# Optimization experiments

Hardware: AMD Instinct MI355X
Metric: run time of the kernel (lower is better)

The kernel has to match this reference:

```python
import jax, jax.numpy as jnp
import numpy as np

V, S, D, H, L = 32000, 2048, 768, 12, 6
HD = D // H
EPS = 1e-5


def _sinusoidal_pe(s, d):
    pos = np.arange(s)[:, None].astype(np.float32)
    div = np.exp(np.arange(0, d, 2).astype(np.float32) * (-np.log(10000.0) / d))
    pe = np.zeros((s, d), dtype=np.float32)
    pe[:, 0::2] = np.sin(pos * div)
    pe[:, 1::2] = np.cos(pos * div)
    return jnp.asarray(pe)


def setup_inputs() -> dict:
    key = jax.random.key(0)
    ks = jax.random.split(key, 16)
    std = 0.02
    tok_emb = jax.random.normal(ks[0], (V, D), jnp.float32) * std
    tok_emb = tok_emb.at[1].set(0.0)  # padding_idx=1
    pos_enc = _sinusoidal_pe(S, D)
    attn_w = jax.random.normal(ks[1], (L, 3 * D, D), jnp.float32) * std
    attn_b = jnp.zeros((L, 3 * D), jnp.float32)
    proj_std = 0.02 / np.sqrt(2 * 6)
    proj_w = jax.random.normal(ks[2], (L, D, D), jnp.float32) * proj_std
    proj_b = jnp.zeros((L, D), jnp.float32)
    ln1_g = jnp.ones((L, D), jnp.float32); ln1_b = jnp.zeros((L, D), jnp.float32)
    ln2_g = jnp.ones((L, D), jnp.float32); ln2_b = jnp.zeros((L, D), jnp.float32)
    fc1_w = jax.random.normal(ks[3], (L, 4 * D, D), jnp.float32) * std
    fc1_b = jnp.zeros((L, 4 * D), jnp.float32)
    fc2_w = jax.random.normal(ks[4], (L, D, 4 * D), jnp.float32) * std
    fc2_b = jnp.zeros((L, D), jnp.float32)
    dec_w = jax.random.normal(ks[5], (V, D), jnp.float32) * std
    idx = jax.random.randint(ks[6], (2, S), 0, V)
    return dict(idx=idx, tok_emb=tok_emb, pos_enc=pos_enc, attn_w=attn_w,
                attn_b=attn_b, proj_w=proj_w, proj_b=proj_b, ln1_g=ln1_g,
                ln1_b=ln1_b, ln2_g=ln2_g, ln2_b=ln2_b, fc1_w=fc1_w,
                fc1_b=fc1_b, fc2_w=fc2_w, fc2_b=fc2_b, dec_w=dec_w)


def _ln(x, g, b):
    mu = jnp.mean(x, -1, keepdims=True)
    var = jnp.mean(jnp.square(x - mu), -1, keepdims=True)
    return (x - mu) * jax.lax.rsqrt(var + EPS) * g + b


def _forward(idx, tok_emb, pos_enc, attn_w, attn_b, proj_w, proj_b,
             ln1_g, ln1_b, ln2_g, ln2_b, fc1_w, fc1_b, fc2_w, fc2_b, dec_w):
    b, s = idx.shape
    x = tok_emb[idx] + pos_enc[:s]  # [b,s,d]
    for l in range(L):
        h = _ln(x, ln1_g[l], ln1_b[l])
        qkv = h @ attn_w[l].T + attn_b[l]
        q, k, v = jnp.split(qkv, 3, axis=-1)
        q = q.reshape(b, s, H, HD).transpose(0, 2, 1, 3)
        k = k.reshape(b, s, H, HD).transpose(0, 2, 1, 3)
        v = v.reshape(b, s, H, HD).transpose(0, 2, 1, 3)
        att = jnp.einsum('bhqd,bhkd->bhqk', q, k) * (1.0 / np.sqrt(HD))
        att = jax.nn.softmax(att, axis=-1)  # no causal mask in source
        y = jnp.einsum('bhqk,bhkd->bhqd', att, v)
        y = y.transpose(0, 2, 1, 3).reshape(b, s, D)
        x = x + (y @ proj_w[l].T + proj_b[l])
        h = _ln(x, ln2_g[l], ln2_b[l])
        h = jax.nn.gelu(h @ fc1_w[l].T + fc1_b[l])
        x = x + (h @ fc2_w[l].T + fc2_b[l])
    return x @ dec_w.T  # [b,s,V]


def reference(idx, tok_emb, pos_enc, attn_w, attn_b, proj_w, proj_b,
              ln1_g, ln1_b, ln2_g, ln2_b, fc1_w, fc1_b, fc2_w, fc2_b, dec_w):
    return _forward(idx, tok_emb, pos_enc, attn_w, attn_b, proj_w, proj_b,
                    ln1_g, ln1_b, ln2_g, ln2_b, fc1_w, fc1_b, fc2_w, fc2_b, dec_w)
```

## Files before the change

### kernel.cpp

```cpp
#include <hip/hip_runtime.h>
#include <hip/hip_bf16.h>
#include <stdint.h>


typedef unsigned short u16;
typedef __attribute__((ext_vector_type(8))) __bf16 bf16x8;
typedef __attribute__((ext_vector_type(4))) float f32x4;
typedef __attribute__((ext_vector_type(4))) unsigned int u32x4;
typedef __attribute__((ext_vector_type(4))) unsigned short u16x4;
typedef __attribute__((ext_vector_type(8))) unsigned short u16x8;

#define MFMA16(a, b, c) __builtin_amdgcn_mfma_f32_16x16x32_bf16((a), (b), (c), 0, 0, 0)

__device__ __forceinline__ float b2f(u16 u) {
  union { unsigned int i; float f; } x; x.i = ((unsigned int)u) << 16; return x.f;
}
__device__ __forceinline__ u16 f2b(float f) {
  union { float f; unsigned int i; } x; x.f = f;
  unsigned int r = x.i + 0x7fffu + ((x.i >> 16) & 1u);
  return (u16)(r >> 16);
}
__device__ __forceinline__ float gelu_f(float v) {
  const float t = 0.7978845608028654f * (v + 0.044715f * v * v * v);
  const float e = __expf(-2.f * fabsf(t));
  float th = (1.f - e) / (1.f + e);
  th = (t < 0.f) ? -th : th;
  return 0.5f * v * (1.f + th);
}
__device__ __forceinline__ void lds16(u16* l, const u16* g) {
  __builtin_amdgcn_global_load_lds(
      (const __attribute__((address_space(1))) unsigned int*)g,
      (__attribute__((address_space(3))) unsigned int*)l, 16, 0, 0);
}

__global__ __launch_bounds__(256) void conv_bf16_kernel(
    const float* __restrict__ src, u16* __restrict__ dst, int n8) {
  int i = blockIdx.x * 256 + threadIdx.x;
  const int stride = gridDim.x * 256;
  for (; i < n8; i += stride) {
    const f32x4 a = *(const f32x4*)&src[(size_t)i * 8];
    const f32x4 b = *(const f32x4*)&src[(size_t)i * 8 + 4];
    u16x8 p;
#pragma unroll
    for (int j = 0; j < 4; ++j) { p[j] = f2b(a[j]); p[4 + j] = f2b(b[j]); }
    *(u16x8*)&dst[(size_t)i * 8] = p;
  }
}

__global__ __launch_bounds__(256) void embed_kernel(
    const int* __restrict__ idx, const float* __restrict__ tok,
    const float* __restrict__ pos, float* __restrict__ x) {
  const int t = blockIdx.x;
  const int s = t & 2047;
  const int tid = threadIdx.x;
  const size_t to = (size_t)idx[t] * 768;
  const size_t po = (size_t)s * 768;
  float* xr = x + (size_t)t * 768;
#pragma unroll
  for (int i = 0; i < 3; ++i) {
    const int d = tid + i * 256;
    xr[d] = tok[to + d] + pos[po + d];
  }
}

__global__ __launch_bounds__(256) void ln_kernel(
    const float* __restrict__ x, const float* __restrict__ g,
    const float* __restrict__ b, u16* __restrict__ out) {
  const int w = threadIdx.x >> 6, lane = threadIdx.x & 63;
  const int row = blockIdx.x * 4 + w;
  const float* xr = x + (size_t)row * 768;
  f32x4 v[3];
#pragma unroll
  for (int i = 0; i < 3; ++i) v[i] = *(const f32x4*)&xr[i * 256 + lane * 4];
  float s = 0.f;
#pragma unroll
  for (int i = 0; i < 3; ++i)
#pragma unroll
    for (int j = 0; j < 4; ++j) s += v[i][j];
#pragma unroll
  for (int m = 1; m < 64; m <<= 1) s += __shfl_xor(s, m);
  const float mu = s * (1.f / 768.f);
  float q = 0.f;
#pragma unroll
  for (int i = 0; i < 3; ++i)
#pragma unroll
    for (int j = 0; j < 4; ++j) {
      const float d = v[i][j] - mu;
      q += d * d;
    }
#pragma unroll
  for (int m = 1; m < 64; m <<= 1) q += __shfl_xor(q, m);
  const float rs = rsqrtf(q * (1.f / 768.f) + 1e-5f);
  u16* orow = out + (size_t)row * 768;
#pragma unroll
  for (int i = 0; i < 3; ++i) {
    const f32x4 gg = *(const f32x4*)&g[i * 256 + lane * 4];
    const f32x4 bb = *(const f32x4*)&b[i * 256 + lane * 4];
    u16x4 o;
#pragma unroll
    for (int j = 0; j < 4; ++j) o[j] = f2b((v[i][j] - mu) * rs * gg[j] + bb[j]);
    *(u16x4*)&orow[i * 256 + lane * 4] = o;
  }
}

#define G8PHASE(H, MH, LOADB)                                                 \
  {                                                                           \
    if (LOADB) {                                                              \
      _Pragma("unroll") for (int n = 0; n < 4; ++n) {                         \
        const int row = wn * 64 + n * 16 + fr;                                \
        bfv[n] = *(const bf16x8*)&Bs_[bufr * 16384 + (H) * 8192 + row * 32 +  \
                                      ((fg ^ ((row ^ (row >> 2)) & 3)) << 3)];\
      }                                                                       \
    }                                                                         \
    bf16x8 af[4];                                                             \
    _Pragma("unroll") for (int m = 0; m < 4; ++m) {                           \
      const int row = wm * 128 + (MH) * 64 + m * 16 + fr;                     \
      af[m] = *(const bf16x8*)&As_[bufr * 16384 + (H) * 8192 + row * 32 +     \
                                   ((fg ^ ((row ^ (row >> 2)) & 3)) << 3)];   \
    }                                                                         \
    __builtin_amdgcn_s_setprio(1);                                            \
    _Pragma("unroll") for (int m = 0; m < 4; ++m)                             \
      _Pragma("unroll") for (int n = 0; n < 4; ++n)                           \
        acc[(MH) * 4 + m][n] = MFMA16(af[m], bfv[n], acc[(MH) * 4 + m][n]);   \
    __builtin_amdgcn_s_setprio(0);                                            \
  }

template <int MODE, int MFAST>
__global__ __launch_bounds__(512, 2) void gemm8(
    const u16* __restrict__ A, const u16* __restrict__ B,
    const float* __restrict__ bias, u16* __restrict__ outb,
    float* __restrict__ outf, float* __restrict__ resid, int N, int K) {
  extern __shared__ u16 sm8[];
  u16* As_ = sm8;
  u16* Bs_ = sm8 + 32768;
  const int tid = threadIdx.x;
  const int lane = tid & 63;
  const int w = tid >> 6;
  const int wm = w >> 2;
  const int wn = w & 3;
  const int fr = lane & 15;
  const int fg = lane >> 4;
  const int bn0 = (MFAST ? blockIdx.y : blockIdx.x) * 256;
  const int bm0 = (MFAST ? blockIdx.x : blockIdx.y) * 256;
  const int nt = K >> 6;

  f32x4 acc[8][4] = {};
  bf16x8 bfv[4];

  auto stage = [&](u16* lbase, const u16* __restrict__ M, int rbase, int k0) {
#pragma unroll
    for (int i = 0; i < 2; ++i) {
      const int c = i * 512 + tid;
      const int row = c >> 2;
      const int slot = (c & 3) ^ ((row ^ (row >> 2)) & 3);
      lds16(lbase + (i * 512 + w * 64) * 8,
            M + (size_t)(rbase + row) * K + k0 + slot * 8);
    }
  };

  stage(As_ + 0, A, bm0, 0);
  stage(Bs_ + 0, B, bn0, 0);
  stage(As_ + 8192, A, bm0, 32);
  stage(Bs_ + 8192, B, bn0, 32);

  int bufr = 0;
  for (int t = 0; t < nt; ++t) {
    const int tn = (t + 1 < nt) ? t + 1 : t;
    const int bufw = bufr ^ 1;
    const int kn = tn * 64;
    asm volatile("s_waitcnt vmcnt(4)" ::: "memory");
    __builtin_amdgcn_sched_barrier(0);
    __builtin_amdgcn_s_barrier();
    stage(As_ + bufw * 16384, A, bm0, kn);
    G8PHASE(0, 0, true)
    stage(Bs_ + bufw * 16384, B, bn0, kn);
    G8PHASE(0, 1, false)
    asm volatile("s_waitcnt vmcnt(4)" ::: "memory");
    __builtin_amdgcn_sched_barrier(0);
    __builtin_amdgcn_s_barrier();
    stage(As_ + bufw * 16384 + 8192, A, bm0, kn + 32);
    G8PHASE(1, 0, true)
    stage(Bs_ + bufw * 16384 + 8192, B, bn0, kn + 32);
    G8PHASE(1, 1, false)
    bufr ^= 1;
  }

#pragma unroll
  for (int n = 0; n < 4; ++n) {
    const int col = bn0 + wn * 64 + n * 16 + fr;
    const float bv = bias ? bias[col] : 0.0f;
#pragma unroll
    for (int i = 0; i < 8; ++i) {
#pragma unroll
      for (int r = 0; r < 4; ++r) {
        const int row = bm0 + wm * 128 + i * 16 + fg * 4 + r;
        float v = acc[i][n][r] + bv;
        if (MODE == 1) v = gelu_f(v);
        const size_t off = (size_t)row * N + col;
        if (MODE == 2) {
          resid[off] += v;
        } else if (MODE == 3) {
          __builtin_nontemporal_store(v, &outf[off]);
        } else {
          outb[off] = f2b(v);
        }
      }
    }
  }
}

template <int MODE, int MFAST>
__global__ __launch_bounds__(256) void gemm_bb(
    const u16* __restrict__ A, const u16* __restrict__ B,
    const float* __restrict__ bias, u16* __restrict__ outb,
    float* __restrict__ outf, float* __restrict__ resid,
    u16* __restrict__ mirror, int N, int K) {
  __shared__ alignas(16) u16 As[2][128 * 64];
  __shared__ alignas(16) u16 Bs[2][128 * 64];
  const int tid = threadIdx.x;
  const int lane = tid & 63;
  const int w = tid >> 6;
  const int wr = (w >> 1) * 64;
  const int wc = (w & 1) * 64;
  const int fr = lane & 15;
  const int fg = lane >> 4;
  const int bn0 = (MFAST ? blockIdx.y : blockIdx.x) * 128;
  const int bm0 = (MFAST ? blockIdx.x : blockIdx.y) * 128;
  const int srow = tid >> 3;

  f32x4 acc[4][4] = {};

  auto stage = [&](int buf, int bk0) {
#pragma unroll
    for (int i = 0; i < 4; ++i) {
      const int row = i * 32 + srow;
      const int slot = (tid & 7) ^ (row & 7);
      lds16(&As[buf][(i * 256 + w * 64) * 8],
            &A[(size_t)(bm0 + row) * K + bk0 + slot * 8]);
      lds16(&Bs[buf][(i * 256 + w * 64) * 8],
            &B[(size_t)(bn0 + row) * K + bk0 + slot * 8]);
    }
  };

  stage(0, 0);
  int cur = 0;
  for (int bk0 = 0; bk0 < K; bk0 += 64) {
    __syncthreads();
    if (bk0 + 64 < K) stage(cur ^ 1, bk0 + 64);
#pragma unroll
    for (int kk = 0; kk < 64; kk += 32) {
      bf16x8 af[4], bfv[4];
#pragma unroll
      for (int m = 0; m < 4; ++m) {
        const int row = wr + m * 16 + fr;
        const int slot = ((kk >> 3) + fg) ^ (row & 7);
        af[m] = *(const bf16x8*)&As[cur][row * 64 + slot * 8];
      }
#pragma unroll
      for (int n = 0; n < 4; ++n) {
        const int row = wc + n * 16 + fr;
        const int slot = ((kk >> 3) + fg) ^ (row & 7);
        bfv[n] = *(const bf16x8*)&Bs[cur][row * 64 + slot * 8];
      }
#pragma unroll
      for (int m = 0; m < 4; ++m)
#pragma unroll
        for (int n = 0; n < 4; ++n)
          acc[m][n] = MFMA16(af[m], bfv[n], acc[m][n]);
    }
    cur ^= 1;
  }

#pragma unroll
  for (int n = 0; n < 4; ++n) {
    const int col = bn0 + wc + n * 16 + fr;
    const float bv = bias ? bias[col] : 0.0f;
#pragma unroll
    for (int m = 0; m < 4; ++m) {
#pragma unroll
      for (int r = 0; r < 4; ++r) {
        const int row = bm0 + wr + m * 16 + fg * 4 + r;
        float v = acc[m][n][r] + bv;
        if (MODE == 1) v = gelu_f(v);
        const size_t off = (size_t)row * N + col;
        if (MODE == 2) {
          const float nv = resid[off] + v;
          resid[off] = nv;
          if (mirror) mirror[off] = f2b(nv);
        } else if (MODE == 3) {
          __builtin_nontemporal_store(v, &outf[off]);
        } else {
          outb[off] = f2b(v);
        }
      }
    }
  }
}

template <int MODE>
__global__ __launch_bounds__(256) void gemm_bt(
    const u16* __restrict__ A, const float* __restrict__ B,
    const float* __restrict__ bias, u16* __restrict__ outb,
    float* __restrict__ outf, float* __restrict__ resid,
    u16* __restrict__ mirror, int N, int K) {
  __shared__ alignas(16) u16 As[128 * 64];
  __shared__ alignas(16) u16 Bs[128 * 64];
  const int tid = threadIdx.x;
  const int lane = tid & 63;
  const int w = tid >> 6;
  const int wr = (w >> 1) * 64;
  const int wc = (w & 1) * 64;
  const int fr = lane & 15;
  const int fg = lane >> 4;
  const int bn0 = blockIdx.x * 128;
  const int bm0 = blockIdx.y * 128;

  f32x4 acc[4][4] = {};

  for (int bk0 = 0; bk0 < K; bk0 += 64) {
    __syncthreads();
#pragma unroll
    for (int i = 0; i < 4; ++i) {
      const int c = i * 256 + tid;
      const int row = c >> 3;
      const int e0 = (c & 7) * 8;
      *(u32x4*)&As[row * 64 + e0] =
          *(const u32x4*)&A[(size_t)(bm0 + row) * K + bk0 + e0];
    }
#pragma unroll
    for (int i = 0; i < 8; ++i) {
      const int c = i * 256 + tid;
      const int row = c >> 4;
      const int e0 = (c & 15) * 4;
      const f32x4 fv = *(const f32x4*)&B[(size_t)(bn0 + row) * K + bk0 + e0];
      u16x4 pv;
#pragma unroll
      for (int j = 0; j < 4; ++j) pv[j] = f2b(fv[j]);
      *(u16x4*)&Bs[row * 64 + e0] = pv;
    }
    __syncthreads();
#pragma unroll
    for (int kk = 0; kk < 64; kk += 32) {
      bf16x8 af[4], bfv[4];
#pragma unroll
      for (int m = 0; m < 4; ++m)
        af[m] = *(const bf16x8*)&As[(wr + m * 16 + fr) * 64 + kk + fg * 8];
#pragma unroll
      for (int n = 0; n < 4; ++n)
        bfv[n] = *(const bf16x8*)&Bs[(wc + n * 16 + fr) * 64 + kk + fg * 8];
#pragma unroll
      for (int m = 0; m < 4; ++m)
#pragma unroll
        for (int n = 0; n < 4; ++n)
          acc[m][n] = MFMA16(af[m], bfv[n], acc[m][n]);
    }
  }

#pragma unroll
  for (int n = 0; n < 4; ++n) {
    const int col = bn0 + wc + n * 16 + fr;
    const float bv = bias ? bias[col] : 0.0f;
#pragma unroll
    for (int m = 0; m < 4; ++m) {
#pragma unroll
      for (int r = 0; r < 4; ++r) {
        const int row = bm0 + wr + m * 16 + fg * 4 + r;
        float v = acc[m][n][r] + bv;
        if (MODE == 1) v = gelu_f(v);
        const size_t off = (size_t)row * N + col;
        if (MODE == 2) {
          const float nv = resid[off] + v;
          resid[off] = nv;
          if (mirror) mirror[off] = f2b(nv);
        } else if (MODE == 3) {
          __builtin_nontemporal_store(v, &outf[off]);
        } else {
          outb[off] = f2b(v);
        }
      }
    }
  }
}

__global__ __launch_bounds__(256) void vtrans_kernel(
    const u16* __restrict__ qkv, u16* __restrict__ vt) {
  __shared__ u16 tile[64][72];
  const int tid = threadIdx.x;
  const int s0 = blockIdx.x * 64;
  const int hh = blockIdx.y;
  const int bb = blockIdx.z;
  const size_t tb = (size_t)bb * 2048 * 2304;
#pragma unroll
  for (int i = 0; i < 2; ++i) {
    const int c = i * 256 + tid;
    const int sl = c >> 3;
    const int d0 = (c & 7) * 8;
    *(u16x8*)&tile[sl][d0] =
        *(const u16x8*)&qkv[tb + (size_t)(s0 + sl) * 2304 + 1536 + hh * 64 + d0];
  }
  __syncthreads();
  const size_t vtb = (size_t)((bb * 12 + hh) * 64) * 2048;
#pragma unroll
  for (int i = 0; i < 2; ++i) {
    const int c = i * 256 + tid;
    const int d = c >> 3;
    const int so = (c & 7) * 8;
    u16x8 p;
#pragma unroll
    for (int j = 0; j < 8; ++j) p[j] = tile[so + j][d];
    *(u16x8*)&vt[vtb + (size_t)d * 2048 + s0 + so] = p;
  }
}

__global__ __launch_bounds__(256) void attn_kernel(
    const u16* __restrict__ qkv, const u16* __restrict__ vt,
    u16* __restrict__ y) {
  __shared__ alignas(16) u16 Ks[2][64 * 64];
  __shared__ alignas(16) u16 VTs[2][64 * 64];
  __shared__ alignas(16) u16 Ps[4][16 * 64];
  const int tid = threadIdx.x;
  const int lane = tid & 63;
  const int w = tid >> 6;
  const int fr = lane & 15;
  const int fg = lane >> 4;
  const int hh = blockIdx.y;
  const int bb = blockIdx.z;
  const size_t tb = (size_t)bb * 2048 * 2304;
  const size_t vtb = (size_t)((bb * 12 + hh) * 64) * 2048;
  const int q0 = blockIdx.x * 64 + w * 16;

  const bf16x8 qf0 =
      *(const bf16x8*)&qkv[tb + (size_t)(q0 + fr) * 2304 + hh * 64 + fg * 8];
  const bf16x8 qf1 =
      *(const bf16x8*)&qkv[tb + (size_t)(q0 + fr) * 2304 + hh * 64 + 32 + fg * 8];

  f32x4 oacc[4] = {};
  float mrow[4] = {-INFINITY, -INFINITY, -INFINITY, -INFINITY};
  float lrow[4] = {0.f, 0.f, 0.f, 0.f};

  const int chunkrow = lane >> 3;
  const int chunkslot = lane & 7;

  auto stage = [&](int buf, int kt) {
#pragma unroll
    for (int i = 0; i < 2; ++i) {
      const int row = (i * 4 + w) * 8 + chunkrow;
      const int slot = chunkslot ^ (row & 7);
      lds16(&Ks[buf][(i * 4 + w) * 512],
            &qkv[tb + (size_t)(kt + row) * 2304 + 768 + hh * 64 + slot * 8]);
      lds16(&VTs[buf][(i * 4 + w) * 512],
            &vt[vtb + (size_t)row * 2048 + kt + slot * 8]);
    }
  };

  stage(0, 0);
  int cur = 0;
  for (int kt = 0; kt < 2048; kt += 64) {
    __syncthreads();
    if (kt + 64 < 2048) stage(cur ^ 1, kt + 64);

    f32x4 s[4] = {};
#pragma unroll
    for (int kb = 0; kb < 4; ++kb) {
      const int row = kb * 16 + fr;
      const int sl0 = (fg) ^ (row & 7);
      const int sl1 = (4 + fg) ^ (row & 7);
      const bf16x8 k0 = *(const bf16x8*)&Ks[cur][row * 64 + sl0 * 8];
      const bf16x8 k1 = *(const bf16x8*)&Ks[cur][row * 64 + sl1 * 8];
      s[kb] = MFMA16(qf0, k0, s[kb]);
      s[kb] = MFMA16(qf1, k1, s[kb]);
    }

    float alpha[4];
    bool anyresc = false;
#pragma unroll
    for (int r = 0; r < 4; ++r) {
      float v[4];
#pragma unroll
      for (int kb = 0; kb < 4; ++kb) v[kb] = s[kb][r] * 0.125f;
      float mx = fmaxf(fmaxf(v[0], v[1]), fmaxf(v[2], v[3]));
      float mn = mrow[r];
      if (__all(mx <= mn)) {
        alpha[r] = 1.f;
      } else {
        mx = fmaxf(mx, __shfl_xor(mx, 1));
        mx = fmaxf(mx, __shfl_xor(mx, 2));
        mx = fmaxf(mx, __shfl_xor(mx, 4));
        mx = fmaxf(mx, __shfl_xor(mx, 8));
        mn = fmaxf(mrow[r], mx);
        alpha[r] = __expf(mrow[r] - mn);
        mrow[r] = mn;
        anyresc = true;
      }
      float p[4];
#pragma unroll
      for (int kb = 0; kb < 4; ++kb) p[kb] = __expf(v[kb] - mn);
      float ps = (p[0] + p[1]) + (p[2] + p[3]);
      ps += __shfl_xor(ps, 1);
      ps += __shfl_xor(ps, 2);
      ps += __shfl_xor(ps, 4);
      ps += __shfl_xor(ps, 8);
      lrow[r] = lrow[r] * alpha[r] + ps;
      const int q = fg * 4 + r;
#pragma unroll
      for (int kb = 0; kb < 4; ++kb) {
        const int kg = kb * 2 + (fr >> 3);
        Ps[w][q * 64 + ((kg ^ (q & 7)) << 3) + (fr & 7)] = f2b(p[kb]);
      }
    }
    if (anyresc) {
#pragma unroll
      for (int db = 0; db < 4; ++db)
#pragma unroll
        for (int r = 0; r < 4; ++r) oacc[db][r] *= alpha[r];
    }

#pragma unroll
    for (int kh = 0; kh < 2; ++kh) {
      const bf16x8 pa =
          *(const bf16x8*)&Ps[w][fr * 64 + (((kh * 4 + fg) ^ (fr & 7)) << 3)];
#pragma unroll
      for (int db = 0; db < 4; ++db) {
        const int row = db * 16 + fr;
        const int slot = (kh * 4 + fg) ^ (row & 7);
        const bf16x8 vb = *(const bf16x8*)&VTs[cur][row * 64 + slot * 8];
        oacc[db] = MFMA16(pa, vb, oacc[db]);
      }
    }
    cur ^= 1;
  }

#pragma unroll
  for (int db = 0; db < 4; ++db) {
#pragma unroll
    for (int r = 0; r < 4; ++r) {
      const int row = q0 + fg * 4 + r;
      y[(size_t)(bb * 2048 + row) * 768 + hh * 64 + db * 16 + fr] =
          f2b(oacc[db][r] / lrow[r]);
    }
  }
}

extern "C" void kernel_launch(void* const* d_in, const int* in_sizes, int n_in,
                              void* d_out, int out_size, void* d_ws,
                              size_t ws_size, hipStream_t stream) {
  const int*   idx   = (const int*)d_in[0];
  const float* tok   = (const float*)d_in[1];
  const float* pos   = (const float*)d_in[2];
  const float* attnw = (const float*)d_in[3];
  const float* attnb = (const float*)d_in[4];
  const float* projw = (const float*)d_in[5];
  const float* projb = (const float*)d_in[6];
  const float* ln1g  = (const float*)d_in[7];
  const float* ln1b  = (const float*)d_in[8];
  const float* ln2g  = (const float*)d_in[9];
  const float* ln2b  = (const float*)d_in[10];
  const float* fc1w  = (const float*)d_in[11];
  const float* fc1b  = (const float*)d_in[12];
  const float* fc2w  = (const float*)d_in[13];
  const float* fc2b  = (const float*)d_in[14];
  const float* decw  = (const float*)d_in[15];

  char* ws = (char*)d_ws;
  float* x = (float*)(ws);
  u16* h   = (u16*)(ws + 12582912);
  u16* qkv = (u16*)(ws + 18874368);
  u16* y   = (u16*)(ws + 37748736);
  u16* h2  = (u16*)(ws + 18874368);
  u16* vt  = h;

  const size_t WB0 = 44040192;
  u16* attnw_b = (u16*)(ws + WB0);
  u16* projw_b = (u16*)(ws + WB0 + 21233664);
  u16* fc1w_b  = (u16*)(ws + WB0 + 28311552);
  u16* fc2w_b  = (u16*)(ws + WB0 + 56623104);
  u16* decw_b  = (u16*)(ws + WB0 + 84934656);
  const size_t NEED = WB0 + 84934656 + 49152000;

  embed_kernel<<<4096, 256, 0, stream>>>(idx, tok, pos, x);

  if (ws_size >= NEED) {
    conv_bf16_kernel<<<2048, 256, 0, stream>>>(attnw, attnw_b, 10616832 / 8);
    conv_bf16_kernel<<<2048, 256, 0, stream>>>(projw, projw_b, 3538944 / 8);
    conv_bf16_kernel<<<2048, 256, 0, stream>>>(fc1w, fc1w_b, 14155776 / 8);
    conv_bf16_kernel<<<2048, 256, 0, stream>>>(fc2w, fc2w_b, 14155776 / 8);
    conv_bf16_kernel<<<2048, 256, 0, stream>>>(decw, decw_b, 24576000 / 8);

    for (int l = 0; l < 6; ++l) {
      ln_kernel<<<1024, 256, 0, stream>>>(x, ln1g + l * 768, ln1b + l * 768, h);
      gemm8<0, 0><<<dim3(9, 16), 512, 131072, stream>>>(
          h, attnw_b + (size_t)l * 2304 * 768, attnb + l * 2304, qkv, nullptr,
          nullptr, 2304, 768);
      vtrans_kernel<<<dim3(32, 12, 2), 256, 0, stream>>>(qkv, vt);
      attn_kernel<<<dim3(32, 12, 2), 256, 0, stream>>>(qkv, vt, y);
      gemm8<2, 0><<<dim3(3, 16), 512, 131072, stream>>>(
          y, projw_b + (size_t)l * 768 * 768, projb + l * 768, nullptr, nullptr,
          x, 768, 768);
      ln_kernel<<<1024, 256, 0, stream>>>(x, ln2g + l * 768, ln2b + l * 768, h);
      gemm8<1, 0><<<dim3(12, 16), 512, 131072, stream>>>(
          h, fc1w_b + (size_t)l * 3072 * 768, fc1b + l * 3072, h2, nullptr,
          nullptr, 3072, 768);
      gemm_bb<2, 0><<<dim3(6, 32), 256, 0, stream>>>(
          h2, fc2w_b + (size_t)l * 768 * 3072, fc2b + l * 768, nullptr, nullptr,
          x, (l == 5) ? h : nullptr, 768, 3072);
    }
    gemm8<3, 1><<<dim3(16, 125), 512, 131072, stream>>>(
        h, decw_b, nullptr, nullptr, (float*)d_out, nullptr, 32000, 768);
  } else {
    for (int l = 0; l < 6; ++l) {
      ln_kernel<<<1024, 256, 0, stream>>>(x, ln1g + l * 768, ln1b + l * 768, h);
      gemm_bt<0><<<dim3(18, 32), 256, 0, stream>>>(
          h, attnw + (size_t)l * 2304 * 768, attnb + l * 2304, qkv, nullptr,
          nullptr, nullptr, 2304, 768);
      vtrans_kernel<<<dim3(32, 12, 2), 256, 0, stream>>>(qkv, vt);
      attn_kernel<<<dim3(32, 12, 2), 256, 0, stream>>>(qkv, vt, y);
      gemm_bt<2><<<dim3(6, 32), 256, 0, stream>>>(
          y, projw + (size_t)l * 768 * 768, projb + l * 768, nullptr, nullptr,
          x, nullptr, 768, 768);
      ln_kernel<<<1024, 256, 0, stream>>>(x, ln2g + l * 768, ln2b + l * 768, h);
      gemm_bt<1><<<dim3(24, 32), 256, 0, stream>>>(
          h, fc1w + (size_t)l * 3072 * 768, fc1b + l * 3072, h2, nullptr,
          nullptr, nullptr, 3072, 768);
      gemm_bt<2><<<dim3(6, 32), 256, 0, stream>>>(
          h2, fc2w + (size_t)l * 768 * 3072, fc2b + l * 768, nullptr, nullptr,
          x, (l == 5) ? h : nullptr, 768, 3072);
    }
    gemm_bt<3><<<dim3(250, 32), 256, 0, stream>>>(
        h, decw, nullptr, nullptr, (float*)d_out, nullptr, nullptr, 32000, 768);
  }
}
```

Measured before the change: 2.006 ms.

## Fuse V-transpose into QKV GEMM, use gemm_bb everywhere, streamline attention softmax

The QKV GEMM now writes the V part directly in transposed layout to a new workspace buffer, so the separate vtrans kernel goes away. The QKV, proj and fc1 GEMMs switch from the 512-thread gemm8 kernel to the smaller 256-thread gemm_bb tile. Attention swaps the MFMA operand order so each lane owns one query row, which removes the cross-lane max and sum reductions, and it packs P with v_cvt_pk_bf16_f32. The five weight conversions are merged into a single launch. Together these cut launch count and softmax overhead, at the cost of a larger workspace requirement and a possibly less efficient GEMM tile.

```diff
diff --git a/kernel.cpp b/kernel.cpp
--- a/kernel.cpp
+++ b/kernel.cpp
@@ -20,6 +20,11 @@
   unsigned int r = x.i + 0x7fffu + ((x.i >> 16) & 1u);
   return (u16)(r >> 16);
 }
+__device__ __forceinline__ unsigned int cvtpk(float lo, float hi) {
+  unsigned int r;
+  asm("v_cvt_pk_bf16_f32 %0, %1, %2" : "=v"(r) : "v"(lo), "v"(hi));
+  return r;
+}
 __device__ __forceinline__ float gelu_f(float v) {
   const float t = 0.7978845608028654f * (v + 0.044715f * v * v * v);
   const float e = __expf(-2.f * fabsf(t));
@@ -33,8 +38,20 @@
       (__attribute__((address_space(3))) unsigned int*)l, 16, 0, 0);
 }
 
-__global__ __launch_bounds__(256) void conv_bf16_kernel(
-    const float* __restrict__ src, u16* __restrict__ dst, int n8) {
+__global__ __launch_bounds__(256) void conv5_kernel(
+    const float* __restrict__ s0, u16* __restrict__ d0, int n0,
+    const float* __restrict__ s1, u16* __restrict__ d1, int n1,
+    const float* __restrict__ s2, u16* __restrict__ d2, int n2,
+    const float* __restrict__ s3, u16* __restrict__ d3, int n3,
+    const float* __restrict__ s4, u16* __restrict__ d4, int n4) {
+  const float* src; u16* dst; int n8;
+  switch (blockIdx.y) {
+    case 0: src = s0; dst = d0; n8 = n0; break;
+    case 1: src = s1; dst = d1; n8 = n1; break;
+    case 2: src = s2; dst = d2; n8 = n2; break;
+    case 3: src = s3; dst = d3; n8 = n3; break;
+    default: src = s4; dst = d4; n8 = n4; break;
+  }
   int i = blockIdx.x * 256 + threadIdx.x;
   const int stride = gridDim.x * 256;
   for (; i < n8; i += stride) {
@@ -100,6 +117,116 @@
 #pragma unroll
     for (int j = 0; j < 4; ++j) o[j] = f2b((v[i][j] - mu) * rs * gg[j] + bb[j]);
     *(u16x4*)&orow[i * 256 + lane * 4] = o;
+  }
+}
+
+template <int MODE, int MFAST>
+__global__ __launch_bounds__(256) void gemm_bb(
+    const u16* __restrict__ A, const u16* __restrict__ B,
+    const float* __restrict__ bias, u16* __restrict__ outb,
+    float* __restrict__ outf, float* __restrict__ resid,
+    u16* __restrict__ mirror, int N, int K) {
+  __shared__ alignas(16) u16 As[2][128 * 64];
+  __shared__ alignas(16) u16 Bs[2][128 * 64];
+  const int tid = threadIdx.x;
+  const int lane = tid & 63;
+  const int w = tid >> 6;
+  const int wr = (w >> 1) * 64;
+  const int wc = (w & 1) * 64;
+  const int fr = lane & 15;
+  const int fg = lane >> 4;
+  const int bn0 = (MFAST ? blockIdx.y : blockIdx.x) * 128;
+  const int bm0 = (MFAST ? blockIdx.x : blockIdx.y) * 128;
+  const int srow = tid >> 3;
+
+  f32x4 acc[4][4] = {};
+
+  auto stage = [&](int buf, int bk0) {
+#pragma unroll
+    for (int i = 0; i < 4; ++i) {
+      const int row = i * 32 + srow;
+      const int slot = (tid & 7) ^ (row & 7);
+      lds16(&As[buf][(i * 256 + w * 64) * 8],
+            &A[(size_t)(bm0 + row) * K + bk0 + slot * 8]);
+      lds16(&Bs[buf][(i * 256 + w * 64) * 8],
+            &B[(size_t)(bn0 + row) * K + bk0 + slot * 8]);
+    }
+  };
+
+  stage(0, 0);
+  int cur = 0;
+  for (int bk0 = 0; bk0 < K; bk0 += 64) {
+    __syncthreads();
+    if (bk0 + 64 < K) stage(cur ^ 1, bk0 + 64);
+#pragma unroll
+    for (int kk = 0; kk < 64; kk += 32) {
+      bf16x8 af[4], bfv[4];
+#pragma unroll
+      for (int m = 0; m < 4; ++m) {
+        const int row = wr + m * 16 + fr;
+        const int slot = ((kk >> 3) + fg) ^ (row & 7);
+        af[m] = *(const bf16x8*)&As[cur][row * 64 + slot * 8];
+      }
+#pragma unroll
+      for (int n = 0; n < 4; ++n) {
+        const int row = wc + n * 16 + fr;
+        const int slot = ((kk >> 3) + fg) ^ (row & 7);
+        bfv[n] = *(const bf16x8*)&Bs[cur][row * 64 + slot * 8];
+      }
+#pragma unroll
+      for (int m = 0; m < 4; ++m)
+#pragma unroll
+        for (int n = 0; n < 4; ++n)
+          acc[m][n] = MFMA16(af[m], bfv[n], acc[m][n]);
+    }
+    cur ^= 1;
+  }
+
+  if (MODE == 4 && bn0 >= 1536) {
+#pragma unroll
+    for (int n = 0; n < 4; ++n) {
+      const int col = bn0 + wc + n * 16 + fr;
+      const float bv = bias[col];
+      const int hcol = col - 1536;
+      const size_t vbase =
+          (size_t)(hcol >> 6) * 64 * 2048 + (size_t)(hcol & 63) * 2048;
+#pragma unroll
+      for (int m = 0; m < 4; ++m) {
+        const int row0 = bm0 + wr + m * 16 + fg * 4;
+        const size_t bboff = (size_t)(row0 >> 11) * 12 * 64 * 2048;
+        const int s = row0 & 2047;
+        u16x4 o;
+#pragma unroll
+        for (int r = 0; r < 4; ++r) o[r] = f2b(acc[m][n][r] + bv);
+        *(u16x4*)&mirror[bboff + vbase + s] = o;
+      }
+    }
+    return;
+  }
+
+#pragma unroll
+  for (int n = 0; n < 4; ++n) {
+    const int col = bn0 + wc + n * 16 + fr;
+    const float bv = bias ? bias[col] : 0.0f;
+#pragma unroll
+    for (int m = 0; m < 4; ++m) {
+#pragma unroll
+      for (int r = 0; r < 4; ++r) {
+        const int row = bm0 + wr + m * 16 + fg * 4 + r;
+        float v = acc[m][n][r] + bv;
+        if (MODE == 1) v = gelu_f(v);
+        const size_t off = (size_t)row * N + col;
+        if (MODE == 2) {
+          const float nv = resid[off] + v;
+          resid[off] = nv;
+          if (mirror) mirror[off] = f2b(nv);
+        } else if (MODE == 3) {
+          __builtin_nontemporal_store(v, &outf[off]);
+        } else {
+          outb[off] = f2b(v);
+        }
+      }
+    }
   }
 }
 
@@ -209,94 +336,6 @@
   }
 }
 
-template <int MODE, int MFAST>
-__global__ __launch_bounds__(256) void gemm_bb(
-    const u16* __restrict__ A, const u16* __restrict__ B,
-    const float* __restrict__ bias, u16* __restrict__ outb,
-    float* __restrict__ outf, float* __restrict__ resid,
-    u16* __restrict__ mirror, int N, int K) {
-  __shared__ alignas(16) u16 As[2][128 * 64];
-  __shared__ alignas(16) u16 Bs[2][128 * 64];
-  const int tid = threadIdx.x;
-  const int lane = tid & 63;
-  const int w = tid >> 6;
-  const int wr = (w >> 1) * 64;
-  const int wc = (w & 1) * 64;
-  const int fr = lane & 15;
-  const int fg = lane >> 4;
-  const int bn0 = (MFAST ? blockIdx.y : blockIdx.x) * 128;
-  const int bm0 = (MFAST ? blockIdx.x : blockIdx.y) * 128;
-  const int srow = tid >> 3;
-
-  f32x4 acc[4][4] = {};
-
-  auto stage = [&](int buf, int bk0) {
-#pragma unroll
-    for (int i = 0; i < 4; ++i) {
-      const int row = i * 32 + srow;
-      const int slot = (tid & 7) ^ (row & 7);
-      lds16(&As[buf][(i * 256 + w * 64) * 8],
-            &A[(size_t)(bm0 + row) * K + bk0 + slot * 8]);
-      lds16(&Bs[buf][(i * 256 + w * 64) * 8],
-            &B[(size_t)(bn0 + row) * K + bk0 + slot * 8]);
-    }
-  };
-
-  stage(0, 0);
-  int cur = 0;
-  for (int bk0 = 0; bk0 < K; bk0 += 64) {
-    __syncthreads();
-    if (bk0 + 64 < K) stage(cur ^ 1, bk0 + 64);
-#pragma unroll
-    for (int kk = 0; kk < 64; kk += 32) {
-      bf16x8 af[4], bfv[4];
-#pragma unroll
-      for (int m = 0; m < 4; ++m) {
-        const int row = wr + m * 16 + fr;
-        const int slot = ((kk >> 3) + fg) ^ (row & 7);
-        af[m] = *(const bf16x8*)&As[cur][row * 64 + slot * 8];
-      }
-#pragma unroll
-      for (int n = 0; n < 4; ++n) {
-        const int row = wc + n * 16 + fr;
-        const int slot = ((kk >> 3) + fg) ^ (row & 7);
-        bfv[n] = *(const bf16x8*)&Bs[cur][row * 64 + slot * 8];
-      }
-#pragma unroll
-      for (int m = 0; m < 4; ++m)
-#pragma unroll
-        for (int n = 0; n < 4; ++n)
-          acc[m][n] = MFMA16(af[m], bfv[n], acc[m][n]);
-    }
-    cur ^= 1;
-  }
-
-#pragma unroll
-  for (int n = 0; n < 4; ++n) {
-    const int col = bn0 + wc + n * 16 + fr;
-    const float bv = bias ? bias[col] : 0.0f;
-#pragma unroll
-    for (int m = 0; m < 4; ++m) {
-#pragma unroll
-      for (int r = 0; r < 4; ++r) {
-        const int row = bm0 + wr + m * 16 + fg * 4 + r;
-        float v = acc[m][n][r] + bv;
-        if (MODE == 1) v = gelu_f(v);
-        const size_t off = (size_t)row * N + col;
-        if (MODE == 2) {
-          const float nv = resid[off] + v;
-          resid[off] = nv;
-          if (mirror) mirror[off] = f2b(nv);
-        } else if (MODE == 3) {
-          __builtin_nontemporal_store(v, &outf[off]);
-        } else {
-          outb[off] = f2b(v);
-        }
-      }
-    }
-  }
-}
-
 template <int MODE>
 __global__ __launch_bounds__(256) void gemm_bt(
     const u16* __restrict__ A, const float* __restrict__ B,
@@ -435,8 +474,7 @@
       *(const bf16x8*)&qkv[tb + (size_t)(q0 + fr) * 2304 + hh * 64 + 32 + fg * 8];
 
   f32x4 oacc[4] = {};
-  float mrow[4] = {-INFINITY, -INFINITY, -INFINITY, -INFINITY};
-  float lrow[4] = {0.f, 0.f, 0.f, 0.f};
+  float m = -INFINITY, l = 0.f;
 
   const int chunkrow = lane >> 3;
   const int chunkslot = lane & 7;
@@ -467,52 +505,63 @@
       const int sl1 = (4 + fg) ^ (row & 7);
       const bf16x8 k0 = *(const bf16x8*)&Ks[cur][row * 64 + sl0 * 8];
       const bf16x8 k1 = *(const bf16x8*)&Ks[cur][row * 64 + sl1 * 8];
-      s[kb] = MFMA16(qf0, k0, s[kb]);
-      s[kb] = MFMA16(qf1, k1, s[kb]);
-    }
-
-    float alpha[4];
-    bool anyresc = false;
-#pragma unroll
-    for (int r = 0; r < 4; ++r) {
-      float v[4];
-#pragma unroll
-      for (int kb = 0; kb < 4; ++kb) v[kb] = s[kb][r] * 0.125f;
-      float mx = fmaxf(fmaxf(v[0], v[1]), fmaxf(v[2], v[3]));
-      float mn = mrow[r];
-      if (__all(mx <= mn)) {
-        alpha[r] = 1.f;
-      } else {
-        mx = fmaxf(mx, __shfl_xor(mx, 1));
-        mx = fmaxf(mx, __shfl_xor(mx, 2));
-        mx = fmaxf(mx, __shfl_xor(mx, 4));
-        mx = fmaxf(mx, __shfl_xor(mx, 8));
-        mn = fmaxf(mrow[r], mx);
-        alpha[r] = __expf(mrow[r] - mn);
-        mrow[r] = mn;
-        anyresc = true;
-      }
-      float p[4];
-#pragma unroll
-      for (int kb = 0; kb < 4; ++kb) p[kb] = __expf(v[kb] - mn);
-      float ps = (p[0] + p[1]) + (p[2] + p[3]);
-      ps += __shfl_xor(ps, 1);
-      ps += __shfl_xor(ps, 2);
-      ps += __shfl_xor(ps, 4);
-      ps += __shfl_xor(ps, 8);
-      lrow[r] = lrow[r] * alpha[r] + ps;
-      const int q = fg * 4 + r;
-#pragma unroll
-      for (int kb = 0; kb < 4; ++kb) {
-        const int kg = kb * 2 + (fr >> 3);
-        Ps[w][q * 64 + ((kg ^ (q & 7)) << 3) + (fr & 7)] = f2b(p[kb]);
-      }
-    }
-    if (anyresc) {
+      s[kb] = MFMA16(k0, qf0, s[kb]);
+      s[kb] = MFMA16(k1, qf1, s[kb]);
+    }
+
+    float v[4][4];
+    float mx = -INFINITY;
+#pragma unroll
+    for (int kb = 0; kb < 4; ++kb)
+#pragma unroll
+      for (int r = 0; r < 4; ++r) {
+        v[kb][r] = s[kb][r] * 0.125f;
+        mx = fmaxf(mx, v[kb][r]);
+      }
+    mx = fmaxf(mx, __shfl_xor(mx, 16));
+    mx = fmaxf(mx, __shfl_xor(mx, 32));
+
+    float alpha = 1.f;
+    const bool resc = !__all(mx <= m);
+    if (resc) {
+      const float mn = fmaxf(m, mx);
+      alpha = __expf(m - mn);
+      m = mn;
+    }
+
+    float ps = 0.f;
+    unsigned int pk[4][2];
+#pragma unroll
+    for (int kb = 0; kb < 4; ++kb) {
+      const float p0 = __expf(v[kb][0] - m);
+      const float p1 = __expf(v[kb][1] - m);
+      const float p2 = __expf(v[kb][2] - m);
+      const float p3 = __expf(v[kb][3] - m);
+      ps += (p0 + p1) + (p2 + p3);
+      pk[kb][0] = cvtpk(p0, p1);
+      pk[kb][1] = cvtpk(p2, p3);
+    }
+    ps += __shfl_xor(ps, 16);
+    ps += __shfl_xor(ps, 32);
+    l = l * alpha + ps;
+
+#pragma unroll
+    for (int kb = 0; kb < 4; ++kb)
+#pragma unroll
+      for (int h = 0; h < 2; ++h) {
+        const int off = fr * 64 + (((2 * kb + (fg >> 1)) ^ (fr & 7)) << 3) +
+                        (2 * (fg & 1) + h) * 2;
+        *(unsigned int*)&Ps[w][off] = pk[kb][h];
+      }
+
+    if (resc) {
+      float alq[4];
+#pragma unroll
+      for (int r = 0; r < 4; ++r) alq[r] = __shfl(alpha, fg * 4 + r);
 #pragma unroll
       for (int db = 0; db < 4; ++db)
 #pragma unroll
-        for (int r = 0; r < 4; ++r) oacc[db][r] *= alpha[r];
+        for (int r = 0; r < 4; ++r) oacc[db][r] *= alq[r];
     }
 
 #pragma unroll
@@ -530,13 +579,16 @@
     cur ^= 1;
   }
 
+  float rq[4];
+#pragma unroll
+  for (int r = 0; r < 4; ++r) rq[r] = 1.0f / __shfl(l, fg * 4 + r);
 #pragma unroll
   for (int db = 0; db < 4; ++db) {
 #pragma unroll
     for (int r = 0; r < 4; ++r) {
       const int row = q0 + fg * 4 + r;
       y[(size_t)(bb * 2048 + row) * 768 + hh * 64 + db * 16 + fr] =
-          f2b(oacc[db][r] / lrow[r]);
+          f2b(oacc[db][r] * rq[r]);
     }
   }
 }
@@ -567,7 +619,6 @@
   u16* qkv = (u16*)(ws + 18874368);
   u16* y   = (u16*)(ws + 37748736);
   u16* h2  = (u16*)(ws + 18874368);
-  u16* vt  = h;
 
   const size_t WB0 = 44040192;
   u16* attnw_b = (u16*)(ws + WB0);
@@ -575,31 +626,30 @@
   u16* fc1w_b  = (u16*)(ws + WB0 + 28311552);
   u16* fc2w_b  = (u16*)(ws + WB0 + 56623104);
   u16* decw_b  = (u16*)(ws + WB0 + 84934656);
-  const size_t NEED = WB0 + 84934656 + 49152000;
+  u16* vt      = (u16*)(ws + WB0 + 84934656 + 49152000);
+  const size_t NEED = WB0 + 84934656 + 49152000 + 12582912;
 
   embed_kernel<<<4096, 256, 0, stream>>>(idx, tok, pos, x);
 
   if (ws_size >= NEED) {
-    conv_bf16_kernel<<<2048, 256, 0, stream>>>(attnw, attnw_b, 10616832 / 8);
-    conv_bf16_kernel<<<2048, 256, 0, stream>>>(projw, projw_b, 3538944 / 8);
-    conv_bf16_kernel<<<2048, 256, 0, stream>>>(fc1w, fc1w_b, 14155776 / 8);
-    conv_bf16_kernel<<<2048, 256, 0, stream>>>(fc2w, fc2w_b, 14155776 / 8);
-    conv_bf16_kernel<<<2048, 256, 0, stream>>>(decw, decw_b, 24576000 / 8);
+    conv5_kernel<<<dim3(1024, 5), 256, 0, stream>>>(
+        attnw, attnw_b, 10616832 / 8, projw, projw_b, 3538944 / 8, fc1w,
+        fc1w_b, 14155776 / 8, fc2w, fc2w_b, 14155776 / 8, decw, decw_b,
+        24576000 / 8);
 
     for (int l = 0; l < 6; ++l) {
       ln_kernel<<<1024, 256, 0, stream>>>(x, ln1g + l * 768, ln1b + l * 768, h);
-      gemm8<0, 0><<<dim3(9, 16), 512, 131072, stream>>>(
+      gemm_bb<4, 0><<<dim3(18, 32), 256, 0, stream>>>(
           h, attnw_b + (size_t)l * 2304 * 768, attnb + l * 2304, qkv, nullptr,
-          nullptr, 2304, 768);
-      vtrans_kernel<<<dim3(32, 12, 2), 256, 0, stream>>>(qkv, vt);
+          nullptr, vt, 2304, 768);
       attn_kernel<<<dim3(32, 12, 2), 256, 0, stream>>>(qkv, vt, y);
-      gemm8<2, 0><<<dim3(3, 16), 512, 131072, stream>>>(
+      gemm_bb<2, 0><<<dim3(6, 32), 256, 0, stream>>>(
           y, projw_b + (size_t)l * 768 * 768, projb + l * 768, nullptr, nullptr,
-          x, 768, 768);
+          x, nullptr, 768, 768);
       ln_kernel<<<1024, 256, 0, stream>>>(x, ln2g + l * 768, ln2b + l * 768, h);
-      gemm8<1, 0><<<dim3(12, 16), 512, 131072, stream>>>(
+      gemm_bb<1, 0><<<dim3(24, 32), 256, 0, stream>>>(
           h, fc1w_b + (size_t)l * 3072 * 768, fc1b + l * 3072, h2, nullptr,
-          nullptr, 3072, 768);
+          nullptr, nullptr, 3072, 768);
       gemm_bb<2, 0><<<dim3(6, 32), 256, 0, stream>>>(
           h2, fc2w_b + (size_t)l * 768 * 3072, fc2b + l * 768, nullptr, nullptr,
           x, (l == 5) ? h : nullptr, 768, 3072);
@@ -612,8 +662,9 @@
       gemm_bt<0><<<dim3(18, 32), 256, 0, stream>>>(
           h, attnw + (size_t)l * 2304 * 768, attnb + l * 2304, qkv, nullptr,
           nullptr, nullptr, 2304, 768);
-      vtrans_kernel<<<dim3(32, 12, 2), 256, 0, stream>>>(qkv, vt);
-      attn_kernel<<<dim3(32, 12, 2), 256, 0, stream>>>(qkv, vt, y);
+      vtrans_kernel<<<dim3(32, 12, 2), 256, 0, stream>>>(qkv, (u16*)(ws + 12582912));
+      attn_kernel<<<dim3(32, 12, 2), 256, 0, stream>>>(
+          qkv, (u16*)(ws + 12582912), y);
       gemm_bt<2><<<dim3(6, 32), 256, 0, stream>>>(
           y, projw + (size_t)l * 768 * 768, projb + l * 768, nullptr, nullptr,
           x, nullptr, 768, 768);
```

Result: faster. 1.814 ms (-9.6%).
